# Kernel tuning notes

Hardware: AMD Instinct MI355X
Metric: run time of the kernel (lower is better)

## Reference

```python
import jax, jax.numpy as jnp
import numpy as np

N, E, D, H, C, G, L = 100000, 1600000, 128, 4, 32, 4096, 3  # nodes, edges, h_dim, heads, head_dim, graphs, conv blocks


def setup_inputs() -> dict:
    key = jax.random.key(0)
    ks = jax.random.split(key, 24)
    s = 0.05
    w = lambda k, shape: jax.random.normal(k, shape, jnp.float32) * s
    inp = {
        "x": jax.random.normal(ks[0], (N, D), jnp.float32),
        "edge_index": jax.random.randint(ks[1], (2, E), 0, N),
        "batch": jnp.sort(jax.random.randint(ks[2], (N,), 0, G)),
        # input TransformerConv (in=D, out=C per head, H heads, beta=True)
        "in_Wq": w(ks[3], (D, D)), "in_bq": jnp.zeros((D,), jnp.float32),
        "in_Wk": w(ks[4], (D, D)), "in_bk": jnp.zeros((D,), jnp.float32),
        "in_Wv": w(ks[5], (D, D)), "in_bv": jnp.zeros((D,), jnp.float32),
        "in_Ws": w(ks[6], (D, D)), "in_bs": jnp.zeros((D,), jnp.float32),
        "in_Wbeta": w(ks[7], (3 * D,)),
        # stacked conv blocks (L of them, in=out=D)
        "blk_Wq": w(ks[8], (L, D, D)), "blk_bq": jnp.zeros((L, D), jnp.float32),
        "blk_Wk": w(ks[9], (L, D, D)), "blk_bk": jnp.zeros((L, D), jnp.float32),
        "blk_Wv": w(ks[10], (L, D, D)), "blk_bv": jnp.zeros((L, D), jnp.float32),
        "blk_Ws": w(ks[11], (L, D, D)), "blk_bs": jnp.zeros((L, D), jnp.float32),
        "blk_Wbeta": w(ks[12], (L, 3 * D)),
        # MLP head
        "W1": w(ks[13], (D, 64)), "b1": jnp.zeros((64,), jnp.float32),
        "W2": w(ks[14], (64, 32)), "b2": jnp.zeros((32,), jnp.float32),
        "W3": w(ks[15], (32, 1)), "b3": jnp.zeros((1,), jnp.float32),
    }
    return inp


def transformer_conv(x, src, dst, Wq, bq, Wk, bk, Wv, bv, Ws, bs, Wbeta):
    # PyG TransformerConv, concat=True, root_weight=True, beta=True, eval mode
    q = (x @ Wq + bq).reshape(N, H, C)
    k = (x @ Wk + bk).reshape(N, H, C)
    v = (x @ Wv + bv).reshape(N, H, C)
    # per-edge attention logits: message j=src -> i=dst
    alpha = jnp.einsum("ehc,ehc->eh", q[dst], k[src]) / jnp.sqrt(jnp.float32(C))  # [E,H]
    m = jax.ops.segment_max(alpha, dst, num_segments=N)
    m = jnp.where(jnp.isfinite(m), m, 0.0)
    e = jnp.exp(alpha - m[dst])
    denom = jax.ops.segment_sum(e, dst, num_segments=N)
    a = e / (denom[dst] + 1e-16)  # segment softmax over in-edges of dst
    msg = a[..., None] * v[src]  # [E,H,C]
    out = jax.ops.segment_sum(msg, dst, num_segments=N).reshape(N, H * C)
    x_r = x @ Ws + bs
    beta = jax.nn.sigmoid(jnp.concatenate([out, x_r, out - x_r], axis=-1) @ Wbeta)[:, None]
    return beta * x_r + (1.0 - beta) * out


def reference(x, edge_index, batch, in_Wq, in_bq, in_Wk, in_bk, in_Wv, in_bv,
              in_Ws, in_bs, in_Wbeta, blk_Wq, blk_bq, blk_Wk, blk_bk, blk_Wv,
              blk_bv, blk_Ws, blk_bs, blk_Wbeta, W1, b1, W2, b2, W3, b3):
    src, dst = edge_index[0], edge_index[1]
    h = jax.nn.relu(transformer_conv(x, src, dst, in_Wq, in_bq, in_Wk, in_bk,
                                     in_Wv, in_bv, in_Ws, in_bs, in_Wbeta))
    for l in range(L):  # dropout is identity in eval mode
        h = jax.nn.relu(transformer_conv(h, src, dst, blk_Wq[l], blk_bq[l],
                                         blk_Wk[l], blk_bk[l], blk_Wv[l], blk_bv[l],
                                         blk_Ws[l], blk_bs[l], blk_Wbeta[l]))
    # global mean pool over graphs
    sums = jax.ops.segment_sum(h, batch, num_segments=G)
    cnt = jax.ops.segment_sum(jnp.ones((N, 1), h.dtype), batch, num_segments=G)
    g = sums / jnp.maximum(cnt, 1.0)
    g = jax.nn.relu(g @ W1 + b1)
    g = jax.nn.relu(g @ W2 + b2)
    return jax.nn.sigmoid(g @ W3 + b3)
```

## Files before the change

### kernel.cpp

```cpp
#include <hip/hip_runtime.h>
#include <hip/hip_bf16.h>
#include <cstdint>

#define DH 128
#define NB 256
#define NBK 1024

typedef __attribute__((ext_vector_type(8))) short short8;
typedef __attribute__((ext_vector_type(4))) float floatx4;
typedef __attribute__((ext_vector_type(2))) float floatx2;

__device__ __forceinline__ float bflo(unsigned u) { return __uint_as_float(u << 16); }
__device__ __forceinline__ float bfhi(unsigned u) { return __uint_as_float(u & 0xffff0000u); }

__device__ __forceinline__ unsigned pk_bf16(float a, float b) {
  return ((unsigned)__bfloat16_as_ushort(__float2bfloat16(b)) << 16)
       | (unsigned)__bfloat16_as_ushort(__float2bfloat16(a));
}

template<int CTRL>
__device__ __forceinline__ float dpp_add(float x) {
  int y = __builtin_amdgcn_update_dpp(0, __float_as_int(x), CTRL, 0xf, 0xf, true);
  return x + __int_as_float(y);
}


__global__ void zero_i32(int* __restrict__ p, int n) {
  int i = blockIdx.x * 256 + threadIdx.x;
  if (i < n) p[i] = 0;
}


__global__ void cvt_bf16(const float* __restrict__ x, __hip_bfloat16* __restrict__ o, int n) {
  int i = blockIdx.x * 256 + threadIdx.x;
  if (i < n) o[i] = __float2bfloat16(x[i]);
}


__global__ void hist_kernel(const int* __restrict__ dst, int* __restrict__ deg, int E) {
  int e = blockIdx.x * 256 + threadIdx.x;
  if (e < E) atomicAdd(&deg[dst[e]], 1);
}

__global__ void scan1_kernel(const int* __restrict__ deg, int* __restrict__ off,
                             int* __restrict__ bsum, int n) {
  __shared__ int sh[256];
  int idx = blockIdx.x * 256 + threadIdx.x;
  int v = (idx < n) ? deg[idx] : 0;
  sh[threadIdx.x] = v;
  __syncthreads();
  for (int d = 1; d < 256; d <<= 1) {
    int x = (threadIdx.x >= (unsigned)d) ? sh[threadIdx.x - d] : 0;
    __syncthreads();
    sh[threadIdx.x] += x;
    __syncthreads();
  }
  if (idx < n) off[idx] = sh[threadIdx.x] - v;
  if (threadIdx.x == 255) bsum[blockIdx.x] = sh[255];
}

__global__ void scan2_kernel(int* __restrict__ bsum, int nb) {
  __shared__ int sh[512];
  int t = threadIdx.x;
  int v = (t < nb) ? bsum[t] : 0;
  sh[t] = v;
  __syncthreads();
  for (int d = 1; d < 512; d <<= 1) {
    int x = (t >= (unsigned)d) ? sh[t - d] : 0;
    __syncthreads();
    sh[t] += x;
    __syncthreads();
  }
  if (t < nb) bsum[t] = sh[t] - v;
}

__global__ void scan3_kernel(int* __restrict__ off, const int* __restrict__ bsum, int n) {
  int idx = blockIdx.x * 256 + threadIdx.x;
  if (idx < n) off[idx] += bsum[blockIdx.x];
}


__global__ __launch_bounds__(256)
void csr_p1(const int* __restrict__ dst, int* __restrict__ hist, int E, int chunk) {
  __shared__ int cnt[NBK];
  const int blk = blockIdx.x, tid = threadIdx.x;
  for (int c = tid; c < NBK; c += 256) cnt[c] = 0;
  __syncthreads();
  int base = blk * chunk;
  int end = base + chunk; if (end > E) end = E;
  for (int e = base + tid; e < end; e += 256) atomicAdd(&cnt[dst[e] >> 7], 1);
  __syncthreads();
  for (int c = tid; c < NBK; c += 256) hist[blk * NBK + c] = cnt[c];
}

__global__ __launch_bounds__(256)
void csr_p2(int* __restrict__ hist, int* __restrict__ total) {
  int b = blockIdx.x * 256 + threadIdx.x;
  int run = 0;
  for (int blk = 0; blk < NB; ++blk) {
    int v = hist[blk * NBK + b];
    hist[blk * NBK + b] = run;
    run += v;
  }
  total[b] = run;
}

__global__ __launch_bounds__(256)
void csr_p3(const int* __restrict__ src, const int* __restrict__ dst,
            const int* __restrict__ hist, const int* __restrict__ tstart,
            int* __restrict__ part, int E, int chunk) {
  __shared__ int cur[NBK];
  const int blk = blockIdx.x, tid = threadIdx.x;
  for (int c = tid; c < NBK; c += 256) cur[c] = hist[blk * NBK + c] + tstart[c];
  __syncthreads();
  int base = blk * chunk;
  int end = base + chunk; if (end > E) end = E;
  for (int e = base + tid; e < end; e += 256) {
    int d = dst[e];
    int b = d >> 7;
    int pos = atomicAdd(&cur[b], 1);
    part[pos] = (src[e] << 7) | (d & 127);
  }
}

__global__ __launch_bounds__(256)
void csr_p4(const int* __restrict__ part, const int* __restrict__ tstart,
            const int* __restrict__ total, int* __restrict__ deg,
            int* __restrict__ off, int* __restrict__ csr, int Nn) {
  __shared__ int lcnt[128], lscan[128], lcur[128];
  const int b = blockIdx.x, tid = threadIdx.x;
  const int p0 = tstart[b];
  const int m = total[b];
  if (tid < 128) lcnt[tid] = 0;
  __syncthreads();
  for (int k = tid; k < m; k += 256) atomicAdd(&lcnt[part[p0 + k] & 127], 1);
  __syncthreads();
  if (tid < 128) lscan[tid] = lcnt[tid];
  __syncthreads();
  for (int d = 1; d < 128; d <<= 1) {
    int v = 0;
    if (tid < 128 && tid >= d) v = lscan[tid - d];
    __syncthreads();
    if (tid < 128) lscan[tid] += v;
    __syncthreads();
  }
  if (tid < 128) {
    int ex = lscan[tid] - lcnt[tid];
    lcur[tid] = ex;
    int n = (b << 7) + tid;
    if (n < Nn) { deg[n] = lcnt[tid]; off[n] = p0 + ex; }
  }
  __syncthreads();
  for (int k = tid; k < m; k += 256) {
    int pk = part[p0 + k];
    int pos = p0 + atomicAdd(&lcur[pk & 127], 1);
    csr[pos] = pk >> 7;
  }
}


__global__ void pack_w_kernel(const float* __restrict__ Wq, const float* __restrict__ Wk,
                              const float* __restrict__ Wv, const float* __restrict__ Ws,
                              const float* __restrict__ bq, const float* __restrict__ bk,
                              const float* __restrict__ bv, const float* __restrict__ bs,
                              __hip_bfloat16* __restrict__ WT, float* __restrict__ bcat) {
  int idx = blockIdx.x * 256 + threadIdx.x;
  if (idx < 512 * DH) {
    int c = idx >> 7, k = idx & 127;
    int which = c >> 7, cc = c & 127;
    const float* W = (which == 0) ? Wq : (which == 1) ? Wk : (which == 2) ? Wv : Ws;
    WT[idx] = __float2bfloat16(W[k * DH + cc]);
    if (k == 0) {
      const float* b = (which == 0) ? bq : (which == 1) ? bk : (which == 2) ? bv : bs;
      bcat[c] = b[cc];
    }
  }
}


__global__ __launch_bounds__(256)
void gemm_qkvs(const short* __restrict__ Xb, const short* __restrict__ WT,
               const float* __restrict__ bc,
               unsigned int* __restrict__ qout,
               unsigned int* __restrict__ kvp,
               unsigned int* __restrict__ xrout, int Nn) {
  const int row0 = blockIdx.x * 64;
  const int tid = threadIdx.x;
  const int w = tid >> 6, lane = tid & 63, quad = lane >> 4, l16 = lane & 15;

  short8 xf[4][4];
#pragma unroll
  for (int nt = 0; nt < 4; ++nt) {
    int node = row0 + nt * 16 + l16; if (node >= Nn) node = Nn - 1;
#pragma unroll
    for (int kt = 0; kt < 4; ++kt)
      xf[nt][kt] = *(const short8*)&Xb[(size_t)node * 128 + kt * 32 + quad * 8];
  }

  if (w == 0 || w == 3) {
    unsigned int* outp = (w == 0) ? qout : xrout;
    const int mbase = (w == 0) ? 0 : 24;
#pragma unroll
    for (int i = 0; i < 8; ++i) {
      const int mt = mbase + i;
      short8 af[4];
#pragma unroll
      for (int kt = 0; kt < 4; ++kt)
        af[kt] = *(const short8*)&WT[(size_t)(mt * 16 + l16) * 128 + kt * 32 + quad * 8];
      float4 bias = *(const float4*)&bc[mt * 16 + quad * 4];
      const int wc = (i * 16 + quad * 4);
#pragma unroll
      for (int nt = 0; nt < 4; ++nt) {
        floatx4 acc = (floatx4){0.f, 0.f, 0.f, 0.f};
#pragma unroll
        for (int kt = 0; kt < 4; ++kt)
          acc = __builtin_amdgcn_mfma_f32_16x16x32_bf16(af[kt], xf[nt][kt], acc, 0, 0, 0);
        int node = row0 + nt * 16 + l16;
        if (node < Nn) {
          uint2 o;
          o.x = pk_bf16(acc[0] + bias.x, acc[1] + bias.y);
          o.y = pk_bf16(acc[2] + bias.z, acc[3] + bias.w);
          *(uint2*)&outp[(size_t)node * 64 + (wc >> 1)] = o;
        }
      }
    }
  } else {
    const int kb = 8 + (w - 1) * 4;
    const int vb = 16 + (w - 1) * 4;
#pragma unroll
    for (int i = 0; i < 4; ++i) {
      const int mk = kb + i, mv = vb + i;
      short8 afk[4], afv[4];
#pragma unroll
      for (int kt = 0; kt < 4; ++kt) {
        afk[kt] = *(const short8*)&WT[(size_t)(mk * 16 + l16) * 128 + kt * 32 + quad * 8];
        afv[kt] = *(const short8*)&WT[(size_t)(mv * 16 + l16) * 128 + kt * 32 + quad * 8];
      }
      float4 bk4 = *(const float4*)&bc[mk * 16 + quad * 4];
      float4 bv4 = *(const float4*)&bc[mv * 16 + quad * 4];
      const int krel = (w - 1) * 64 + i * 16 + quad * 4;
#pragma unroll
      for (int nt = 0; nt < 4; ++nt) {
        floatx4 ak = (floatx4){0.f, 0.f, 0.f, 0.f};
        floatx4 av = (floatx4){0.f, 0.f, 0.f, 0.f};
#pragma unroll
        for (int kt = 0; kt < 4; ++kt) {
          ak = __builtin_amdgcn_mfma_f32_16x16x32_bf16(afk[kt], xf[nt][kt], ak, 0, 0, 0);
          av = __builtin_amdgcn_mfma_f32_16x16x32_bf16(afv[kt], xf[nt][kt], av, 0, 0, 0);
        }
        int node = row0 + nt * 16 + l16;
        if (node < Nn) {
          int d0 = __builtin_amdgcn_cvt_pk_fp8_f32(ak[0] + bk4.x, ak[1] + bk4.y, 0, false);
          d0 = __builtin_amdgcn_cvt_pk_fp8_f32(av[0] + bv4.x, av[1] + bv4.y, d0, true);
          int d1 = __builtin_amdgcn_cvt_pk_fp8_f32(ak[2] + bk4.z, ak[3] + bk4.w, 0, false);
          d1 = __builtin_amdgcn_cvt_pk_fp8_f32(av[2] + bv4.z, av[3] + bv4.w, d1, true);
          uint2 o; o.x = (unsigned)d0; o.y = (unsigned)d1;
          *(uint2*)&kvp[(size_t)node * 64 + (krel >> 1)] = o;
        }
      }
    }
  }
}


__global__ __launch_bounds__(256)
void attn_kernel(unsigned int* __restrict__ q_h, const unsigned int* __restrict__ kvp,
                 const unsigned int* __restrict__ xrb, const int* __restrict__ off,
                 const int* __restrict__ deg, const int* __restrict__ csr,
                 const float* __restrict__ Wb, int Nn) {
  int wv = __builtin_amdgcn_readfirstlane(threadIdx.x >> 6);
  int i = blockIdx.x * 4 + wv;
  if (i >= Nn) return;
  int l = threadIdx.x & 63;

  unsigned qp = q_h[(size_t)i * 64 + l];
  float q0 = bflo(qp), q1 = bfhi(qp);
  int e0 = off[i], e1 = e0 + deg[i];

  float den0 = 0.f, x00 = 0.f, x10 = 0.f;
  float den1 = 0.f, x01 = 0.f, x11 = 0.f;
  float den2 = 0.f, x02 = 0.f, x12 = 0.f;
  float den3 = 0.f, x03 = 0.f, x13 = 0.f;

  auto body = [&](int e, float& den, float& a0, float& a1) {
    int s = csr[e];
    int kq = (int)kvp[(size_t)s * 64 + l];
    floatx2 kk = __builtin_amdgcn_cvt_pk_f32_fp8(kq, false);
    floatx2 vv = __builtin_amdgcn_cvt_pk_f32_fp8(kq, true);
    float d = q0 * kk.x + q1 * kk.y;
    d = dpp_add<0x128>(d);
    d = dpp_add<0x124>(d);
    d = dpp_add<0x122>(d);
    d = dpp_add<0x121>(d);
    float p = __expf(d * 0.17677669529663687f);
    den += p; a0 += p * vv.x; a1 += p * vv.y;
  };

  int e = e0;
  for (; e + 3 < e1; e += 4) {
    body(e + 0, den0, x00, x10);
    body(e + 1, den1, x01, x11);
    body(e + 2, den2, x02, x12);
    body(e + 3, den3, x03, x13);
  }
  for (; e < e1; ++e) body(e, den0, x00, x10);

  float denom = den0 + den1 + den2 + den3 + 1e-16f;
  float o0 = (x00 + x01 + x02 + x03) / denom;
  float o1 = (x10 + x11 + x12 + x13) / denom;

  unsigned xp = xrb[(size_t)i * 64 + l];
  float xr0 = bflo(xp), xr1 = bfhi(xp);

  float c = o0 * Wb[2 * l] + o1 * Wb[2 * l + 1]
          + xr0 * Wb[128 + 2 * l] + xr1 * Wb[128 + 2 * l + 1]
          + (o0 - xr0) * Wb[256 + 2 * l] + (o1 - xr1) * Wb[256 + 2 * l + 1];
  c += __shfl_xor(c, 1);
  c += __shfl_xor(c, 2);
  c += __shfl_xor(c, 4);
  c += __shfl_xor(c, 8);
  c += __shfl_xor(c, 16);
  c += __shfl_xor(c, 32);
  float beta = 1.f / (1.f + __expf(-c));
  float h0 = fmaxf(beta * xr0 + (1.f - beta) * o0, 0.f);
  float h1 = fmaxf(beta * xr1 + (1.f - beta) * o1, 0.f);
  q_h[(size_t)i * 64 + l] = pk_bf16(h0, h1);
}


__global__ __launch_bounds__(128)
void poolmlp_kernel(const unsigned short* __restrict__ h, const int* __restrict__ goff,
                    const int* __restrict__ gdeg,
                    const float* __restrict__ W1, const float* __restrict__ b1,
                    const float* __restrict__ W2, const float* __restrict__ b2,
                    const float* __restrict__ W3, const float* __restrict__ b3,
                    float* __restrict__ out) {
  int g = blockIdx.x;
  int t = threadIdx.x;
  int n0 = goff[g], cnt = gdeg[g];
  float s = 0.f;
  for (int n = n0; n < n0 + cnt; ++n) s += bflo(h[(size_t)n * 128 + t]);
  __shared__ float gv[128];
  __shared__ float t1[64];
  __shared__ float t2[32];
  gv[t] = s / fmaxf((float)cnt, 1.0f);
  __syncthreads();
  if (t < 64) {
    float a = b1[t];
    for (int k = 0; k < 128; ++k) a += gv[k] * W1[k * 64 + t];
    t1[t] = fmaxf(a, 0.f);
  }
  __syncthreads();
  if (t < 32) {
    float a = b2[t];
    for (int k = 0; k < 64; ++k) a += t1[k] * W2[k * 32 + t];
    t2[t] = fmaxf(a, 0.f);
  }
  __syncthreads();
  if (t == 0) {
    float a = b3[0];
    for (int k = 0; k < 32; ++k) a += t2[k] * W3[k];
    out[g] = 1.f / (1.f + __expf(-a));
  }
}


extern "C" void kernel_launch(void* const* d_in, const int* in_sizes, int n_in,
                              void* d_out, int out_size, void* d_ws, size_t ws_size,
                              hipStream_t stream) {
  const float* x = (const float*)d_in[0];
  const int* edge_index = (const int*)d_in[1];
  const int* batch = (const int*)d_in[2];
  const int N = in_sizes[0] / DH;
  const int E = in_sizes[1] / 2;
  const int G = out_size;
  const int* src = edge_index;
  const int* dst = edge_index + E;

  const float* in_Wq = (const float*)d_in[3];
  const float* in_bq = (const float*)d_in[4];
  const float* in_Wk = (const float*)d_in[5];
  const float* in_bk = (const float*)d_in[6];
  const float* in_Wv = (const float*)d_in[7];
  const float* in_bv = (const float*)d_in[8];
  const float* in_Ws = (const float*)d_in[9];
  const float* in_bs = (const float*)d_in[10];
  const float* in_Wbeta = (const float*)d_in[11];
  const float* blk_Wq = (const float*)d_in[12];
  const float* blk_bq = (const float*)d_in[13];
  const float* blk_Wk = (const float*)d_in[14];
  const float* blk_bk = (const float*)d_in[15];
  const float* blk_Wv = (const float*)d_in[16];
  const float* blk_bv = (const float*)d_in[17];
  const float* blk_Ws = (const float*)d_in[18];
  const float* blk_bs = (const float*)d_in[19];
  const float* blk_Wbeta = (const float*)d_in[20];

  char* p = (char*)d_ws;
  auto take = [&](size_t bytes) { char* r = p; p += (bytes + 255) & ~(size_t)255; return r; };
  __hip_bfloat16* h0 = (__hip_bfloat16*)take((size_t)N * DH * 2);
  __hip_bfloat16* h1 = (__hip_bfloat16*)take((size_t)N * DH * 2);
  unsigned char* kvp = (unsigned char*)take((size_t)N * 256);
  unsigned short* xr = (unsigned short*)take((size_t)N * DH * 2);
  __hip_bfloat16* WT = (__hip_bfloat16*)take((size_t)512 * DH * 2);
  float* bcat = (float*)take(512 * 4);
  int* deg    = (int*)take((size_t)N * 4);
  int* off    = (int*)take((size_t)N * 4);
  int* csr    = (int*)take((size_t)E * 4);
  int* part   = (int*)take((size_t)E * 4);
  int* hist   = (int*)take((size_t)NB * NBK * 4);
  int* total  = (int*)take(NBK * 4);
  int* tstart = (int*)take(NBK * 4);
  int* bsumP  = (int*)take(512 * 4);
  int* gdeg   = (int*)take((size_t)G * 4);
  int* goff   = (int*)take((size_t)G * 4);
  int* bsum2  = (int*)take(512 * 4);
  (void)n_in;
  if ((size_t)(p - (char*)d_ws) > ws_size) return;

  const int NBUCK = (N + 127) >> 7;
  const int chunk = (E + NB - 1) / NB;
  int nb = (N + 255) / 256;
  int gb = (G + 255) / 256;

  csr_p1<<<NB, 256, 0, stream>>>(dst, hist, E, chunk);
  csr_p2<<<NBK / 256, 256, 0, stream>>>(hist, total);
  scan1_kernel<<<NBK / 256, 256, 0, stream>>>(total, tstart, bsumP, NBK);
  scan2_kernel<<<1, 512, 0, stream>>>(bsumP, NBK / 256);
  scan3_kernel<<<NBK / 256, 256, 0, stream>>>(tstart, bsumP, NBK);
  csr_p3<<<NB, 256, 0, stream>>>(src, dst, hist, tstart, part, E, chunk);
  csr_p4<<<NBUCK, 256, 0, stream>>>(part, tstart, total, deg, off, csr, N);

  zero_i32<<<gb, 256, 0, stream>>>(gdeg, G);
  hist_kernel<<<nb, 256, 0, stream>>>(batch, gdeg, N);
  scan1_kernel<<<gb, 256, 0, stream>>>(gdeg, goff, bsum2, G);
  scan2_kernel<<<1, 512, 0, stream>>>(bsum2, gb);
  scan3_kernel<<<gb, 256, 0, stream>>>(goff, bsum2, G);

  cvt_bf16<<<(int)(((size_t)N * DH + 255) / 256), 256, 0, stream>>>(x, h0, N * DH);

  for (int l = 0; l < 4; ++l) {
    const float *Wq, *Wk, *Wv, *Ws, *bq, *bk, *bv, *bs, *Wb;
    if (l == 0) {
      Wq = in_Wq; Wk = in_Wk; Wv = in_Wv; Ws = in_Ws;
      bq = in_bq; bk = in_bk; bv = in_bv; bs = in_bs; Wb = in_Wbeta;
    } else {
      int m = l - 1;
      Wq = blk_Wq + (size_t)m * DH * DH; Wk = blk_Wk + (size_t)m * DH * DH;
      Wv = blk_Wv + (size_t)m * DH * DH; Ws = blk_Ws + (size_t)m * DH * DH;
      bq = blk_bq + (size_t)m * DH; bk = blk_bk + (size_t)m * DH;
      bv = blk_bv + (size_t)m * DH; bs = blk_bs + (size_t)m * DH;
      Wb = blk_Wbeta + (size_t)m * 3 * DH;
    }
    __hip_bfloat16* hin  = (l & 1) ? h1 : h0;
    __hip_bfloat16* qbuf = (l & 1) ? h0 : h1;
    pack_w_kernel<<<(512 * DH + 255) / 256, 256, 0, stream>>>(Wq, Wk, Wv, Ws, bq, bk, bv, bs, WT, bcat);
    gemm_qkvs<<<(N + 63) / 64, 256, 0, stream>>>((const short*)hin, (const short*)WT, bcat,
        (unsigned int*)qbuf, (unsigned int*)kvp, (unsigned int*)xr, N);
    attn_kernel<<<(N + 3) / 4, 256, 0, stream>>>((unsigned int*)qbuf, (const unsigned int*)kvp,
        (const unsigned int*)xr, off, deg, csr, Wb, N);
  }

  poolmlp_kernel<<<G, 128, 0, stream>>>((const unsigned short*)h0, goff, gdeg,
      (const float*)d_in[21], (const float*)d_in[22],
      (const float*)d_in[23], (const float*)d_in[24],
      (const float*)d_in[25], (const float*)d_in[26],
      (float*)d_out);
}
```

Measured before the change: 790.2 us.

## Streamline preprocessing: transposed hist scan, binary-search graph offsets, tiled weight pack

The per-block bucket histogram is stored transposed so csr_p2 can scan each bucket with one wave using vector loads and shuffles. Five kernels that built graph offsets (zero, atomic histogram, three-pass scan) are replaced by one binary-search kernel over the sorted batch array. The weight pack now transposes through a shared-memory tile for coalesced access, and the attention kernel computes the kv index with 32-bit math. These aim to cut launch count and uncoalesced traffic in small setup kernels. The binary search relies on batch being sorted, which the task guarantees.

```diff
diff --git a/kernel.cpp b/kernel.cpp
--- a/kernel.cpp
+++ b/kernel.cpp
@@ -25,22 +25,11 @@
 }
 
 
-__global__ void zero_i32(int* __restrict__ p, int n) {
-  int i = blockIdx.x * 256 + threadIdx.x;
-  if (i < n) p[i] = 0;
-}
-
-
 __global__ void cvt_bf16(const float* __restrict__ x, __hip_bfloat16* __restrict__ o, int n) {
   int i = blockIdx.x * 256 + threadIdx.x;
   if (i < n) o[i] = __float2bfloat16(x[i]);
 }
 
-
-__global__ void hist_kernel(const int* __restrict__ dst, int* __restrict__ deg, int E) {
-  int e = blockIdx.x * 256 + threadIdx.x;
-  if (e < E) atomicAdd(&deg[dst[e]], 1);
-}
 
 __global__ void scan1_kernel(const int* __restrict__ deg, int* __restrict__ off,
                              int* __restrict__ bsum, int n) {
@@ -90,19 +79,29 @@
   int end = base + chunk; if (end > E) end = E;
   for (int e = base + tid; e < end; e += 256) atomicAdd(&cnt[dst[e] >> 7], 1);
   __syncthreads();
-  for (int c = tid; c < NBK; c += 256) hist[blk * NBK + c] = cnt[c];
-}
+  for (int c = tid; c < NBK; c += 256) hist[c * NB + blk] = cnt[c];
+}
+
 
 __global__ __launch_bounds__(256)
 void csr_p2(int* __restrict__ hist, int* __restrict__ total) {
-  int b = blockIdx.x * 256 + threadIdx.x;
-  int run = 0;
-  for (int blk = 0; blk < NB; ++blk) {
-    int v = hist[blk * NBK + b];
-    hist[blk * NBK + b] = run;
-    run += v;
-  }
-  total[b] = run;
+  int b = blockIdx.x * 4 + (threadIdx.x >> 6);
+  int lane = threadIdx.x & 63;
+  int4 v = *(int4*)&hist[b * NB + lane * 4];
+  int s0 = v.x;
+  int s1 = s0 + v.y;
+  int s2 = s1 + v.z;
+  int s3 = s2 + v.w;
+  int t = s3;
+  for (int d = 1; d < 64; d <<= 1) {
+    int y = __shfl_up(t, d);
+    if (lane >= d) t += y;
+  }
+  int excl = t - s3;
+  int4 o;
+  o.x = excl; o.y = excl + s0; o.z = excl + s1; o.w = excl + s2;
+  *(int4*)&hist[b * NB + lane * 4] = o;
+  if (lane == 63) total[b] = t;
 }
 
 __global__ __launch_bounds__(256)
@@ -111,7 +110,7 @@
             int* __restrict__ part, int E, int chunk) {
   __shared__ int cur[NBK];
   const int blk = blockIdx.x, tid = threadIdx.x;
-  for (int c = tid; c < NBK; c += 256) cur[c] = hist[blk * NBK + c] + tstart[c];
+  for (int c = tid; c < NBK; c += 256) cur[c] = hist[c * NB + blk] + tstart[c];
   __syncthreads();
   int base = blk * chunk;
   int end = base + chunk; if (end > E) end = E;
@@ -159,22 +158,43 @@
 }
 
 
-__global__ void pack_w_kernel(const float* __restrict__ Wq, const float* __restrict__ Wk,
-                              const float* __restrict__ Wv, const float* __restrict__ Ws,
-                              const float* __restrict__ bq, const float* __restrict__ bk,
-                              const float* __restrict__ bv, const float* __restrict__ bs,
-                              __hip_bfloat16* __restrict__ WT, float* __restrict__ bcat) {
-  int idx = blockIdx.x * 256 + threadIdx.x;
-  if (idx < 512 * DH) {
-    int c = idx >> 7, k = idx & 127;
-    int which = c >> 7, cc = c & 127;
-    const float* W = (which == 0) ? Wq : (which == 1) ? Wk : (which == 2) ? Wv : Ws;
-    WT[idx] = __float2bfloat16(W[k * DH + cc]);
-    if (k == 0) {
+__global__ void goff_kernel(const int* __restrict__ batch, int* __restrict__ goff,
+                            int N, int G) {
+  int g = blockIdx.x * 256 + threadIdx.x;
+  if (g > G) return;
+  if (g == G) { goff[G] = N; return; }
+  int lo = 0, hi = N;
+  while (lo < hi) { int mid = (lo + hi) >> 1; if (batch[mid] < g) lo = mid + 1; else hi = mid; }
+  goff[g] = lo;
+}
+
+
+__global__ __launch_bounds__(256)
+void pack_w_kernel(const float* __restrict__ Wq, const float* __restrict__ Wk,
+                   const float* __restrict__ Wv, const float* __restrict__ Ws,
+                   const float* __restrict__ bq, const float* __restrict__ bk,
+                   const float* __restrict__ bv, const float* __restrict__ bs,
+                   __hip_bfloat16* __restrict__ WT, float* __restrict__ bcat) {
+  if (blockIdx.x == 64) {
+    for (int c = threadIdx.x; c < 512; c += 256) {
+      int which = c >> 7, cc = c & 127;
       const float* b = (which == 0) ? bq : (which == 1) ? bk : (which == 2) ? bv : bs;
       bcat[c] = b[cc];
     }
-  }
+    return;
+  }
+  __shared__ float tile[32][33];
+  const int bid = blockIdx.x;
+  const int which = bid >> 4, kb = (bid >> 2) & 3, cb = bid & 3;
+  const float* W = (which == 0) ? Wq : (which == 1) ? Wk : (which == 2) ? Wv : Ws;
+  const int tx = threadIdx.x & 31, ty = threadIdx.x >> 5;
+#pragma unroll
+  for (int r = ty; r < 32; r += 8)
+    tile[r][tx] = W[(kb * 32 + r) * 128 + cb * 32 + tx];
+  __syncthreads();
+#pragma unroll
+  for (int r = ty; r < 32; r += 8)
+    WT[(size_t)(which * 128 + cb * 32 + r) * 128 + kb * 32 + tx] = __float2bfloat16(tile[tx][r]);
 }
 
 
@@ -284,7 +304,7 @@
 
   auto body = [&](int e, float& den, float& a0, float& a1) {
     int s = csr[e];
-    int kq = (int)kvp[(size_t)s * 64 + l];
+    int kq = (int)kvp[(s << 6) | l];
     floatx2 kk = __builtin_amdgcn_cvt_pk_f32_fp8(kq, false);
     floatx2 vv = __builtin_amdgcn_cvt_pk_f32_fp8(kq, true);
     float d = q0 * kk.x + q1 * kk.y;
@@ -330,14 +350,13 @@
 
 __global__ __launch_bounds__(128)
 void poolmlp_kernel(const unsigned short* __restrict__ h, const int* __restrict__ goff,
-                    const int* __restrict__ gdeg,
                     const float* __restrict__ W1, const float* __restrict__ b1,
                     const float* __restrict__ W2, const float* __restrict__ b2,
                     const float* __restrict__ W3, const float* __restrict__ b3,
                     float* __restrict__ out) {
   int g = blockIdx.x;
   int t = threadIdx.x;
-  int n0 = goff[g], cnt = gdeg[g];
+  int n0 = goff[g], cnt = goff[g + 1] - n0;
   float s = 0.f;
   for (int n = n0; n < n0 + cnt; ++n) s += bflo(h[(size_t)n * 128 + t]);
   __shared__ float gv[128];
@@ -412,30 +431,22 @@
   int* total  = (int*)take(NBK * 4);
   int* tstart = (int*)take(NBK * 4);
   int* bsumP  = (int*)take(512 * 4);
-  int* gdeg   = (int*)take((size_t)G * 4);
-  int* goff   = (int*)take((size_t)G * 4);
-  int* bsum2  = (int*)take(512 * 4);
+  int* goff   = (int*)take((size_t)(G + 1) * 4);
   (void)n_in;
   if ((size_t)(p - (char*)d_ws) > ws_size) return;
 
   const int NBUCK = (N + 127) >> 7;
   const int chunk = (E + NB - 1) / NB;
-  int nb = (N + 255) / 256;
-  int gb = (G + 255) / 256;
 
   csr_p1<<<NB, 256, 0, stream>>>(dst, hist, E, chunk);
-  csr_p2<<<NBK / 256, 256, 0, stream>>>(hist, total);
+  csr_p2<<<NBK / 4, 256, 0, stream>>>(hist, total);
   scan1_kernel<<<NBK / 256, 256, 0, stream>>>(total, tstart, bsumP, NBK);
   scan2_kernel<<<1, 512, 0, stream>>>(bsumP, NBK / 256);
   scan3_kernel<<<NBK / 256, 256, 0, stream>>>(tstart, bsumP, NBK);
   csr_p3<<<NB, 256, 0, stream>>>(src, dst, hist, tstart, part, E, chunk);
   csr_p4<<<NBUCK, 256, 0, stream>>>(part, tstart, total, deg, off, csr, N);
 
-  zero_i32<<<gb, 256, 0, stream>>>(gdeg, G);
-  hist_kernel<<<nb, 256, 0, stream>>>(batch, gdeg, N);
-  scan1_kernel<<<gb, 256, 0, stream>>>(gdeg, goff, bsum2, G);
-  scan2_kernel<<<1, 512, 0, stream>>>(bsum2, gb);
-  scan3_kernel<<<gb, 256, 0, stream>>>(goff, bsum2, G);
+  goff_kernel<<<(G + 256) / 256, 256, 0, stream>>>(batch, goff, N, G);
 
   cvt_bf16<<<(int)(((size_t)N * DH + 255) / 256), 256, 0, stream>>>(x, h0, N * DH);
 
@@ -454,14 +465,14 @@
     }
     __hip_bfloat16* hin  = (l & 1) ? h1 : h0;
     __hip_bfloat16* qbuf = (l & 1) ? h0 : h1;
-    pack_w_kernel<<<(512 * DH + 255) / 256, 256, 0, stream>>>(Wq, Wk, Wv, Ws, bq, bk, bv, bs, WT, bcat);
+    pack_w_kernel<<<65, 256, 0, stream>>>(Wq, Wk, Wv, Ws, bq, bk, bv, bs, WT, bcat);
     gemm_qkvs<<<(N + 63) / 64, 256, 0, stream>>>((const short*)hin, (const short*)WT, bcat,
         (unsigned int*)qbuf, (unsigned int*)kvp, (unsigned int*)xr, N);
     attn_kernel<<<(N + 3) / 4, 256, 0, stream>>>((unsigned int*)qbuf, (const unsigned int*)kvp,
         (const unsigned int*)xr, off, deg, csr, Wb, N);
   }
 
-  poolmlp_kernel<<<G, 128, 0, stream>>>((const unsigned short*)h0, goff, gdeg,
+  poolmlp_kernel<<<G, 128, 0, stream>>>((const unsigned short*)h0, goff,
       (const float*)d_in[21], (const float*)d_in[22],
       (const float*)d_in[23], (const float*)d_in[24],
       (const float*)d_in[25], (const float*)d_in[26],
```

Result: no change. 784.4 us (-0.7%).
